# Kernel tuning notes

Hardware: AMD Instinct MI355X
Metric: run time of the kernel (lower is better)

The kernel has to match this reference:

```python
import jax, jax.numpy as jnp
import numpy as np

KERNEL = (7, 7)
NUM_CH = 4
EPS = 1e-06
ROPE_BASE = 10000.0


def _rel_dist():
    coords = [np.arange(k, dtype=np.float32) - k // 2 for k in KERNEL]
    g = np.meshgrid(*coords, indexing='ij')
    d = np.sqrt(sum(gi ** 2 for gi in g))
    return jnp.asarray(d.reshape(-1)), float(d.max())


def silu(x):
    return x * jax.nn.sigmoid(x)


def rmsnorm(x, w):
    rms = jnp.sqrt(jnp.mean(x * x, axis=-1, keepdims=True) + EPS)
    return x / rms * w


def apply_rope(x):
    # x: (B, L, H, D); positions run over dim -2 (matches torch default)
    H, D = x.shape[-2], x.shape[-1]
    half = D // 2
    pos = jnp.arange(H, dtype=jnp.float32)
    freqs = 1.0 / (ROPE_BASE ** (jnp.arange(half, dtype=x.dtype) / half))
    ang = pos[:, None] * freqs  # (H, half)
    cos, sin = jnp.cos(ang), jnp.sin(ang)
    x1, x2 = x[..., :half], x[..., half:2 * half]
    return jnp.concatenate([x1 * cos - x2 * sin, x1 * sin + x2 * cos], axis=-1)


def unfold2d(x):
    # x: (B, Hs, Ws, C) -> (B, Hs, Ws, k1*k2, C), row-major kernel order
    B, Hs, Ws, C = x.shape
    k1, k2 = KERNEL
    xp = jnp.pad(x, ((0, 0), ((k1 - 1) // 2, k1 // 2), ((k2 - 1) // 2, k2 // 2), (0, 0)))
    wins = [xp[:, i:i + Hs, j:j + Ws, :] for i in range(k1) for j in range(k2)]
    return jnp.stack(wins, axis=3)


def setup_inputs() -> dict:
    key = jax.random.key(0)
    ks = jax.random.split(key, 8)
    C = 256
    x = jax.random.normal(ks[0], (2, 64, 64, C), dtype=jnp.float32)
    W_qkv = jax.random.normal(ks[1], (C, 3 * C), dtype=jnp.float32) * 0.02
    w_qnorm = jnp.ones((C // NUM_CH,), dtype=jnp.float32)
    w_knorm = jnp.ones((C // NUM_CH,), dtype=jnp.float32)
    W_wp = jax.random.normal(ks[2], (C, 2 * NUM_CH), dtype=jnp.float32) * 0.02
    b_wp = jax.random.normal(ks[3], (2 * NUM_CH,), dtype=jnp.float32) * 0.02
    w_onorm = jnp.ones((C,), dtype=jnp.float32)
    W_out = jax.random.normal(ks[4], (C, C), dtype=jnp.float32) * 0.02
    W_gate = jax.random.normal(ks[5], (C, C), dtype=jnp.float32) * 0.02
    b_gate = 2.0 * jnp.ones((C,), dtype=jnp.float32)
    return {"x": x, "W_qkv": W_qkv, "w_qnorm": w_qnorm, "w_knorm": w_knorm,
            "W_wp": W_wp, "b_wp": b_wp, "w_onorm": w_onorm, "W_out": W_out,
            "W_gate": W_gate, "b_gate": b_gate}


def reference(x, W_qkv, w_qnorm, w_knorm, W_wp, b_wp, w_onorm, W_out, W_gate, b_gate):
    rel_dist, max_dist = _rel_dist()
    B, Hs, Ws, C = x.shape
    L = Hs * Ws
    H = NUM_CH
    D = C // H
    Wsz = KERNEL[0] * KERNEL[1]
    scale = D ** (-0.5)

    qkv = silu(x @ W_qkv)
    q, k, v = jnp.split(qkv, 3, axis=-1)

    q_flat = apply_rope(rmsnorm(q.reshape(B, L, H, D), w_qnorm))
    k_flat = apply_rope(rmsnorm(k.reshape(B, L, H, D), w_knorm))
    k = k_flat.reshape(B, Hs, Ws, C)

    wp = silu(x @ W_wp + b_wp)  # (B, Hs, Ws, 2H)
    width_raw, sharp_raw = jnp.split(wp, 2, axis=-1)
    width = jax.nn.sigmoid(width_raw) * max_dist + 0.5
    sharpness = jax.nn.sigmoid(sharp_raw) * 9.5 + 0.5

    k_win = unfold2d(k).reshape(B, L, Wsz, H, D)
    v_win = unfold2d(v).reshape(B, L, Wsz, H, D)

    scores = jnp.einsum('blhd,blwhd->blhw', q_flat, k_win) * scale
    width_f = width.reshape(B, L, H, 1)
    sharp_f = sharpness.reshape(B, L, H, 1)
    soft_mask = jax.nn.sigmoid((width_f - rel_dist) * sharp_f)
    scores = scores - (1.0 - soft_mask) * 10000.0
    attn = jax.nn.softmax(scores, axis=-1)

    out = jnp.einsum('blhw,blwhd->blhd', attn, v_win).reshape(B, Hs, Ws, C)
    out = rmsnorm(out, w_onorm)

    gate = jax.nn.sigmoid(silu(v @ W_gate + b_gate))
    merged = gate * v + (1.0 - gate) * out
    return silu(merged @ W_out)
```

## Files before the change

kernel.cpp:

```cpp
#include <hip/hip_runtime.h>
#include <hip/hip_fp16.h>
#include <math.h>

__device__ __forceinline__ float sigm(float x)  { return 1.0f / (1.0f + __expf(-x)); }
__device__ __forceinline__ float siluf(float x) { return x * sigm(x); }

typedef _Float16 half8  __attribute__((ext_vector_type(8)));
typedef _Float16 half4  __attribute__((ext_vector_type(4)));
typedef float    f32x4  __attribute__((ext_vector_type(4)));

__device__ __forceinline__ void gld16(const void* g, void* l) {
    __builtin_amdgcn_global_load_lds(
        (const __attribute__((address_space(1))) unsigned*)g,
        (__attribute__((address_space(3))) unsigned*)l, 16, 0, 0);
}

template <int MI, int AMODE>
__device__ __forceinline__ void gemm_core16(
    const __half* __restrict__ A16,
    const __half* __restrict__ Bhi, const __half* __restrict__ Blo,
    int nbs, int m0, int n0, int t, f32x4 (&acc)[MI][4])
{
    __shared__ short As[MI * 1024], BsHi[4096], BsLo[4096];
    const int lane = t & 63, wave = t >> 6;
    const int wm = (wave >> 1) * (MI << 4), wn = (wave & 1) << 6;
    const int fr = lane & 15, fq = lane >> 4;

    for (int kb = 0; kb < 8; ++kb) {
        __syncthreads();
#pragma unroll
        for (int hf = 0; hf < MI / 2; ++hf) {
            const int rr = wave * (MI << 3) + (hf << 4);
            size_t ga;
            if (AMODE == 0)
                ga = (((size_t)(kb * 8192 + m0 + rr)) << 5) + (lane << 3);
            else
                ga = (((size_t)(m0 + rr + (lane >> 2))) << 8) + (kb << 5) + ((lane & 3) << 3);
            gld16(A16 + ga, &As[rr << 5]);
        }
#pragma unroll
        for (int hf = 0; hf < 2; ++hf) {
            const int rr = (wave << 5) + (hf << 4);
            const size_t gb = (((size_t)(kb * nbs + n0 + rr)) << 5) + (lane << 3);
            gld16(Bhi + gb, &BsHi[rr << 5]);
            gld16(Blo + gb, &BsLo[rr << 5]);
        }
        __syncthreads();

        half8 a[MI], bh[4], bl[4];
#pragma unroll
        for (int i = 0; i < MI; ++i)
            a[i] = *(const half8*)&As[((wm + (i << 4) + fr) << 5) + (fq << 3)];
#pragma unroll
        for (int i = 0; i < 4; ++i) {
            const int boff = ((wn + (i << 4) + fr) << 5) + (fq << 3);
            bh[i] = *(const half8*)&BsHi[boff];
            bl[i] = *(const half8*)&BsLo[boff];
        }
#pragma unroll
        for (int mi = 0; mi < MI; ++mi)
#pragma unroll
            for (int ni = 0; ni < 4; ++ni) {
                acc[mi][ni] = __builtin_amdgcn_mfma_f32_16x16x32_f16(a[mi], bh[ni], acc[mi][ni], 0, 0, 0);
                acc[mi][ni] = __builtin_amdgcn_mfma_f32_16x16x32_f16(a[mi], bl[ni], acc[mi][ni], 0, 0, 0);
            }
    }
}

__global__ __launch_bounds__(256) void prep_kernel(
    const float* __restrict__ x, const float* __restrict__ Wqkv,
    const float* __restrict__ Wgate, const float* __restrict__ Wout,
    const float* __restrict__ Wwp, const float* __restrict__ bwp,
    __half* __restrict__ xh,
    __half* __restrict__ wqh, __half* __restrict__ wql,
    __half* __restrict__ wgh, __half* __restrict__ wgl,
    __half* __restrict__ woh, __half* __restrict__ wol,
    float* __restrict__ width, float* __restrict__ sharp)
{
    __shared__ float xs[32][260];
    const int t = threadIdx.x;
    const int blk = blockIdx.x;
    if (blk < 256) {
        const int row0 = blk << 5;
        for (int e = t; e < 2048; e += 256) {
            int r = e >> 6, cc = (e & 63) << 2;
            *(float4*)&xs[r][cc] = *(const float4*)&x[(size_t)(row0 + r) * 256 + cc];
        }
        __syncthreads();
        const int r = t >> 3, kb = t & 7;
        __half hibuf[32];
#pragma unroll
        for (int i = 0; i < 32; ++i)
            hibuf[i] = __float2half(xs[r][(kb << 5) + i]);
        const size_t ob = ((size_t)(kb * 8192 + row0 + r)) << 5;
#pragma unroll
        for (int i = 0; i < 4; ++i)
            *(int4*)&xh[ob + (i << 3)] = *(int4*)&hibuf[i << 3];
        float acc = 0.f;
#pragma unroll 8
        for (int k = 0; k < 256; ++k) acc += xs[r][k] * Wwp[k * 8 + kb];
        float s = sigm(siluf(acc + bwp[kb]));
        const int row = row0 + r;
        if (kb < 4) width[row * 4 + kb] = s * 4.242640687119285f + 0.5f;
        else        sharp[row * 4 + kb - 4] = s * 9.5f + 0.5f;
    } else {
        const float* W; __half *Whi, *Wlo; int N, nb0, ncnt;
        if (blk < 288)      { W = Wqkv;  Whi = wqh; Wlo = wql; N = 768; nb0 = (blk - 256) * 24; ncnt = 24; }
        else if (blk < 296) { W = Wgate; Whi = wgh; Wlo = wgl; N = 256; nb0 = (blk - 288) * 32; ncnt = 32; }
        else                { W = Wout;  Whi = woh; Wlo = wol; N = 256; nb0 = (blk - 296) * 32; ncnt = 32; }
        for (int j = 0; j < ncnt; ++j)
            xs[j][t] = W[(size_t)t * N + nb0 + j];
        __syncthreads();
        for (int c = t; c < ncnt * 8; c += 256) {
            const int j = c >> 3, kb = c & 7;
            __half hibuf[32], lobuf[32];
#pragma unroll
            for (int i = 0; i < 32; ++i) {
                float v = xs[j][(kb << 5) + i];
                __half hv = __float2half(v);
                hibuf[i] = hv;
                lobuf[i] = __float2half(v - __half2float(hv));
            }
            const size_t ob = ((size_t)(kb * N + nb0 + j)) << 5;
#pragma unroll
            for (int i = 0; i < 4; ++i) {
                *(int4*)&Whi[ob + (i << 3)] = *(int4*)&hibuf[i << 3];
                *(int4*)&Wlo[ob + (i << 3)] = *(int4*)&lobuf[i << 3];
            }
        }
    }
}

__global__ __launch_bounds__(256, 3) void gemm_qkv(
    const __half* __restrict__ xh,
    const __half* __restrict__ wqh, const __half* __restrict__ wql,
    const float* __restrict__ wq, const float* __restrict__ wk,
    __half* __restrict__ qh, __half* __restrict__ kh, __half* __restrict__ vh)
{
    const int t  = threadIdx.x;
    const int m0 = blockIdx.y << 7, n0 = blockIdx.x << 7;
    f32x4 acc[4][4] = {};
    gemm_core16<4, 0>(xh, wqh, wql, 768, m0, n0, t, acc);

    const int lane = t & 63, wave = t >> 6;
    const int wm = (wave >> 1) << 6, wn = (wave & 1) << 6;
    const int fr = lane & 15, fq = lane >> 4;
    const int gc0 = n0 + wn;
    const int seg = gc0 >> 8;
    const int h   = (gc0 >> 6) & 3;
    const int hc0 = h << 6;

#pragma unroll
    for (int mi = 0; mi < 4; ++mi)
#pragma unroll
        for (int ni = 0; ni < 4; ++ni)
#pragma unroll
            for (int r = 0; r < 4; ++r)
                acc[mi][ni][r] = siluf(acc[mi][ni][r]);

    if (seg == 2) {
#pragma unroll
        for (int mi = 0; mi < 4; ++mi)
#pragma unroll
            for (int r = 0; r < 4; ++r) {
                const size_t row = m0 + wm + (mi << 4) + (fq << 2) + r;
#pragma unroll
                for (int ni = 0; ni < 4; ++ni)
                    vh[row * 256 + hc0 + (ni << 4) + fr] = __float2half(acc[mi][ni][r]);
            }
    } else {
        const float* wnorm = seg ? wk : wq;
        float wv[4];
#pragma unroll
        for (int ni = 0; ni < 4; ++ni) wv[ni] = wnorm[(ni << 4) + fr];
        float cs[2], sn[2];
#pragma unroll
        for (int j = 0; j < 2; ++j) {
            const int d = (j << 4) + fr;
            const float freq = powf(10000.f, -(float)d * (1.f / 32.f));
            const float ang = (float)h * freq;
            cs[j] = cosf(ang); sn[j] = sinf(ang);
        }
        __half* dstbase = (seg ? kh : qh);
#pragma unroll
        for (int mi = 0; mi < 4; ++mi)
#pragma unroll
            for (int r = 0; r < 4; ++r) {
                float ss = acc[mi][0][r] * acc[mi][0][r] + acc[mi][1][r] * acc[mi][1][r]
                         + acc[mi][2][r] * acc[mi][2][r] + acc[mi][3][r] * acc[mi][3][r];
                ss += __shfl_xor(ss, 1); ss += __shfl_xor(ss, 2);
                ss += __shfl_xor(ss, 4); ss += __shfl_xor(ss, 8);
                const float rinv = 1.f / sqrtf(ss * (1.f / 64.f) + 1e-6f);
                float xv[4];
#pragma unroll
                for (int ni = 0; ni < 4; ++ni) xv[ni] = acc[mi][ni][r] * rinv * wv[ni];
                const float o0 = xv[0] * cs[0] - xv[2] * sn[0];
                const float o2 = xv[0] * sn[0] + xv[2] * cs[0];
                const float o1 = xv[1] * cs[1] - xv[3] * sn[1];
                const float o3 = xv[1] * sn[1] + xv[3] * cs[1];
                const size_t row = m0 + wm + (mi << 4) + (fq << 2) + r;
                __half* dst = dstbase + row * 256 + hc0;
                dst[fr]      = __float2half(o0);
                dst[16 + fr] = __float2half(o1);
                dst[32 + fr] = __float2half(o2);
                dst[48 + fr] = __float2half(o3);
            }
    }
}

__global__ __launch_bounds__(256, 3) void gemm_gate(
    const __half* __restrict__ vh,
    const __half* __restrict__ wgh, const __half* __restrict__ wgl,
    const float* __restrict__ bias, const float* __restrict__ attn_o,
    const float* __restrict__ sumsq4, const float* __restrict__ w_onorm,
    __half* __restrict__ mh)
{
    const int t  = threadIdx.x;
    const int m0 = blockIdx.y << 6, n0 = blockIdx.x << 7;
    f32x4 acc[2][4] = {};
    gemm_core16<2, 1>(vh, wgh, wgl, 256, m0, n0, t, acc);

    const int lane = t & 63, wave = t >> 6;
    const int wm = (wave >> 1) << 5, wn = (wave & 1) << 6;
    const int fr = lane & 15, fq = lane >> 4;

    float rmsf[2][4];
#pragma unroll
    for (int mi = 0; mi < 2; ++mi)
#pragma unroll
        for (int r = 0; r < 4; ++r) {
            const int m = m0 + wm + (mi << 4) + (fq << 2) + r;
            float4 s4 = *(const float4*)&sumsq4[(size_t)m * 4];
            rmsf[mi][r] = 1.f / sqrtf((s4.x + s4.y + s4.z + s4.w) * (1.f / 256.f) + 1e-6f);
        }

#pragma unroll
    for (int mi = 0; mi < 2; ++mi)
#pragma unroll
        for (int ni = 0; ni < 4; ++ni) {
            const int n  = n0 + wn + (ni << 4) + fr;
            const int mb = m0 + wm + (mi << 4) + (fq << 2);
            const float bb  = bias[n];
            const float won = w_onorm[n];
#pragma unroll
            for (int r = 0; r < 4; ++r) {
                const int m = mb + r;
                const float g  = sigm(siluf(acc[mi][ni][r] + bb));
                const float vv = __half2float(vh[(size_t)m * 256 + n]);
                const float oo = attn_o[(size_t)m * 256 + n] * rmsf[mi][r] * won;
                mh[(size_t)m * 256 + n] = __float2half(g * vv + (1.f - g) * oo);
            }
        }
}

__global__ __launch_bounds__(256, 3) void gemm_out(
    const __half* __restrict__ mh,
    const __half* __restrict__ woh, const __half* __restrict__ wol,
    float* __restrict__ out)
{
    const int t  = threadIdx.x;
    const int m0 = blockIdx.y << 6, n0 = blockIdx.x << 7;
    f32x4 acc[2][4] = {};
    gemm_core16<2, 1>(mh, woh, wol, 256, m0, n0, t, acc);

    const int lane = t & 63, wave = t >> 6;
    const int wm = (wave >> 1) << 5, wn = (wave & 1) << 6;
    const int fr = lane & 15, fq = lane >> 4;
#pragma unroll
    for (int mi = 0; mi < 2; ++mi)
#pragma unroll
        for (int ni = 0; ni < 4; ++ni) {
            const int n  = n0 + wn + (ni << 4) + fr;
            const int mb = m0 + wm + (mi << 4) + (fq << 2);
#pragma unroll
            for (int r = 0; r < 4; ++r)
                out[(size_t)(mb + r) * 256 + n] = siluf(acc[mi][ni][r]);
        }
}

#define PTV 208
#define PTP 112

__global__ __launch_bounds__(256, 4) void attn_mfma(
    const __half* __restrict__ qh, const __half* __restrict__ kh,
    const __half* __restrict__ vh, const float* __restrict__ width,
    const float* __restrict__ sharp, float* __restrict__ attn_o,
    float* __restrict__ sumsq4)
{
    __shared__ short smem[20480];
    short* Vt  = smem;
    short* Psh = smem + 13312;

    const int t = threadIdx.x;
    const int lane = t & 63, wave = t >> 6;
    const int fr = lane & 15, fq = lane >> 4;
    const int patch = blockIdx.x, h = blockIdx.y, b = blockIdx.z;
    const int pr0 = (patch >> 3) << 3, pc0 = (patch & 7) << 3;
    const size_t cb0 = ((size_t)b << 20) + ((size_t)h << 6);

    float wd[4], sh[4]; int lq[4];
#pragma unroll
    for (int r = 0; r < 4; ++r) {
        const int q = (wave << 4) + (fq << 2) + r;
        lq[r] = (pr0 + (q >> 3)) * 64 + pc0 + (q & 7);
        wd[r] = width[((b << 12) + lq[r]) * 4 + h];
        sh[r] = sharp[((b << 12) + lq[r]) * 4 + h];
    }

    const int srow = t >> 5;
    const int d2 = (t & 31) << 1;
    unsigned v0[13], v1[13];
#pragma unroll
    for (int j = 0; j < 13; ++j) {
        const int p = (j << 4) + (srow << 1);
#pragma unroll
        for (int e = 0; e < 2; ++e) {
            const int pp = p + e;
            const int pi = pp / 14, pj = pp - pi * 14;
            const int gr = pr0 - 3 + pi, gc = pc0 - 3 + pj;
            const bool ok = (pp < 196) & ((unsigned)gr < 64u) & ((unsigned)gc < 64u);
            const int grc = min(max(gr, 0), 63), gcc = min(max(gc, 0), 63);
            const unsigned vv = *(const unsigned*)(vh + cb0 + (size_t)((grc << 6) + gcc) * 256 + d2);
            (e ? v1 : v0)[j] = ok ? vv : 0u;
        }
    }
#pragma unroll
    for (int j = 0; j < 13; ++j) {
        const int p = (j << 4) + (srow << 1);
        const unsigned lo = (v0[j] & 0xffffu) | (v1[j] << 16);
        const unsigned hi = (v0[j] >> 16) | (v1[j] & 0xffff0000u);
        *(unsigned*)&Vt[d2 * PTV + p]       = lo;
        *(unsigned*)&Vt[(d2 + 1) * PTV + p] = hi;
    }

    const int qrow = (wave << 4) + fr;
    const int lqr = (pr0 + (qrow >> 3)) * 64 + pc0 + (qrow & 7);
    const __half* qptr = qh + cb0 + (size_t)lqr * 256 + (fq << 3);
    half8 a0 = *(const half8*)qptr;
    half8 a1 = *(const half8*)(qptr + 32);

    f32x4 sc[13];
#define KADDR(tl) ({                                                        \
        const int p_ = ((tl) << 4) + fr;                                    \
        const int pi_ = p_ / 14, pj_ = p_ - pi_ * 14;                       \
        const int grc_ = min(max(pr0 - 3 + pi_, 0), 63);                    \
        const int gcc_ = min(max(pc0 - 3 + pj_, 0), 63);                    \
        kh + cb0 + (size_t)((grc_ << 6) + gcc_) * 256 + (fq << 3); })

    half8 k0a[5], k0b[5];
#pragma unroll
    for (int i = 0; i < 5; ++i) {
        const __half* kp = KADDR(i);
        k0a[i] = *(const half8*)kp; k0b[i] = *(const half8*)(kp + 32);
    }
    half8 k1a[4], k1b[4];
#pragma unroll
    for (int i = 0; i < 4; ++i) {
        const __half* kp = KADDR(5 + i);
        k1a[i] = *(const half8*)kp; k1b[i] = *(const half8*)(kp + 32);
    }
#pragma unroll
    for (int i = 0; i < 5; ++i) {
        f32x4 z = {0.f, 0.f, 0.f, 0.f};
        z = __builtin_amdgcn_mfma_f32_16x16x32_f16(a0, k0a[i], z, 0, 0, 0);
        sc[i] = __builtin_amdgcn_mfma_f32_16x16x32_f16(a1, k0b[i], z, 0, 0, 0);
    }
    half8 k2a[4], k2b[4];
#pragma unroll
    for (int i = 0; i < 4; ++i) {
        const __half* kp = KADDR(9 + i);
        k2a[i] = *(const half8*)kp; k2b[i] = *(const half8*)(kp + 32);
    }
#pragma unroll
    for (int i = 0; i < 4; ++i) {
        f32x4 z = {0.f, 0.f, 0.f, 0.f};
        z = __builtin_amdgcn_mfma_f32_16x16x32_f16(a0, k1a[i], z, 0, 0, 0);
        sc[5 + i] = __builtin_amdgcn_mfma_f32_16x16x32_f16(a1, k1b[i], z, 0, 0, 0);
    }
#pragma unroll
    for (int i = 0; i < 4; ++i) {
        f32x4 z = {0.f, 0.f, 0.f, 0.f};
        z = __builtin_amdgcn_mfma_f32_16x16x32_f16(a0, k2a[i], z, 0, 0, 0);
        sc[9 + i] = __builtin_amdgcn_mfma_f32_16x16x32_f16(a1, k2b[i], z, 0, 0, 0);
    }
#undef KADDR

    float mx[4] = {-3e38f, -3e38f, -3e38f, -3e38f};
#pragma unroll
    for (int tl = 0; tl < 13; ++tl) {
        const int p = (tl << 4) + fr;
        const int pi = p / 14, pj = p - pi * 14;
        const bool pvld = p < 196;
        const bool inb = pvld & ((unsigned)(pr0 - 3 + pi) < 64u) & ((unsigned)(pc0 - 3 + pj) < 64u);
#pragma unroll
        for (int r = 0; r < 4; ++r) {
            const int q = (wave << 4) + (fq << 2) + r;
            const int di = pi - 3 - ((q >> 3) & 7), dj = pj - 3 - (q & 7);
            const bool win = pvld & ((unsigned)(di + 3) <= 6u) & ((unsigned)(dj + 3) <= 6u);
            const float rel = sqrtf((float)(di * di + dj * dj));
            const float mk = sigm((wd[r] - rel) * sh[r]);
            const float s0 = inb ? sc[tl][r] * 0.125f : 0.f;
            float s = s0 - (1.f - mk) * 10000.f;
            s = win ? s : -3e38f;
            sc[tl][r] = s;
            mx[r] = fmaxf(mx[r], s);
        }
    }
#pragma unroll
    for (int r = 0; r < 4; ++r) {
        mx[r] = fmaxf(mx[r], __shfl_xor(mx[r], 1));
        mx[r] = fmaxf(mx[r], __shfl_xor(mx[r], 2));
        mx[r] = fmaxf(mx[r], __shfl_xor(mx[r], 4));
        mx[r] = fmaxf(mx[r], __shfl_xor(mx[r], 8));
    }
    float sm[4] = {0.f, 0.f, 0.f, 0.f};
#pragma unroll
    for (int tl = 0; tl < 13; ++tl)
#pragma unroll
        for (int r = 0; r < 4; ++r) {
            const float e = __expf(sc[tl][r] - mx[r]);
            sc[tl][r] = e; sm[r] += e;
        }
#pragma unroll
    for (int r = 0; r < 4; ++r) {
        sm[r] += __shfl_xor(sm[r], 1);
        sm[r] += __shfl_xor(sm[r], 2);
        sm[r] += __shfl_xor(sm[r], 4);
        sm[r] += __shfl_xor(sm[r], 8);
        sm[r] = 1.f / sm[r];
    }

#pragma unroll
    for (int tl = 0; tl < 7; ++tl)
#pragma unroll
        for (int r = 0; r < 4; ++r) {
            __half pv = __float2half(sc[tl][r] * sm[r]);
            Psh[((wave << 4) + (fq << 2) + r) * PTP + (tl << 4) + fr] = *(short*)&pv;
        }
    __syncthreads();

    f32x4 o[4] = {};
    const int pra = (wave << 4) + fr;
#pragma unroll
    for (int s = 0; s < 3; ++s) {
        half8 pa = *(const half8*)&Psh[pra * PTP + (fq << 3) + (s << 5)];
#pragma unroll
        for (int dt = 0; dt < 4; ++dt) {
            half8 vbf = *(const half8*)&Vt[((dt << 4) + fr) * PTV + (fq << 3) + (s << 5)];
            o[dt] = __builtin_amdgcn_mfma_f32_16x16x32_f16(pa, vbf, o[dt], 0, 0, 0);
        }
    }
    {
        half4 pa = *(const half4*)&Psh[pra * PTP + 96 + (fq << 2)];
#pragma unroll
        for (int dt = 0; dt < 4; ++dt) {
            half4 vbf = *(const half4*)&Vt[((dt << 4) + fr) * PTV + 96 + (fq << 2)];
            o[dt] = __builtin_amdgcn_mfma_f32_16x16x16f16(pa, vbf, o[dt], 0, 0, 0);
        }
    }

    __syncthreads();

#pragma unroll
    for (int tl = 7; tl < 13; ++tl)
#pragma unroll
        for (int r = 0; r < 4; ++r) {
            __half pv = __float2half(sc[tl][r] * sm[r]);
            Psh[((wave << 4) + (fq << 2) + r) * PTP + ((tl - 7) << 4) + fr] = *(short*)&pv;
        }
    asm volatile("s_waitcnt lgkmcnt(0)" ::: "memory");

#pragma unroll
    for (int s = 0; s < 3; ++s) {
        half8 pa = *(const half8*)&Psh[pra * PTP + (fq << 3) + (s << 5)];
#pragma unroll
        for (int dt = 0; dt < 4; ++dt) {
            half8 vbf = *(const half8*)&Vt[((dt << 4) + fr) * PTV + 112 + (fq << 3) + (s << 5)];
            o[dt] = __builtin_amdgcn_mfma_f32_16x16x32_f16(pa, vbf, o[dt], 0, 0, 0);
        }
    }

#pragma unroll
    for (int r = 0; r < 4; ++r) {
        float ss = o[0][r]*o[0][r] + o[1][r]*o[1][r] + o[2][r]*o[2][r] + o[3][r]*o[3][r];
        ss += __shfl_xor(ss, 1); ss += __shfl_xor(ss, 2);
        ss += __shfl_xor(ss, 4); ss += __shfl_xor(ss, 8);
        const size_t rowb = (((size_t)(b << 12) + lq[r]) << 8) + h * 64;
#pragma unroll
        for (int dt = 0; dt < 4; ++dt)
            attn_o[rowb + (dt << 4) + fr] = o[dt][r];
        if (fr == 0) sumsq4[(((b << 12) + lq[r]) << 2) + h] = ss;
    }
}

extern "C" void kernel_launch(void* const* d_in, const int* in_sizes, int n_in,
                              void* d_out, int out_size, void* d_ws, size_t ws_size,
                              hipStream_t stream)
{
    const float* x      = (const float*)d_in[0];
    const float* W_qkv  = (const float*)d_in[1];
    const float* w_qn   = (const float*)d_in[2];
    const float* w_kn   = (const float*)d_in[3];
    const float* W_wp   = (const float*)d_in[4];
    const float* b_wp   = (const float*)d_in[5];
    const float* w_on   = (const float*)d_in[6];
    const float* W_out  = (const float*)d_in[7];
    const float* W_gate = (const float*)d_in[8];
    const float* b_gate = (const float*)d_in[9];
    float* out = (float*)d_out;

    __half* ws16 = (__half*)d_ws;
    __half* xh  = ws16;
    __half* wqh = xh  + 2097152;
    __half* wql = wqh + 196608;
    __half* wgh = wql + 196608;
    __half* wgl = wgh + 65536;
    __half* woh = wgl + 65536;
    __half* wol = woh + 65536;
    __half* qhp = wol + 65536;
    __half* khp = qhp + 2097152;
    __half* vhp = khp + 2097152;
    __half* mh  = vhp + 2097152;
    float* attn_o = (float*)(mh + 2097152);
    float* widthp = attn_o + 2097152;
    float* sharpp = widthp + 32768;
    float* sumsq4 = sharpp + 32768;

    prep_kernel<<<304, 256, 0, stream>>>(x, W_qkv, W_gate, W_out, W_wp, b_wp,
                                         xh, wqh, wql, wgh, wgl, woh, wol,
                                         widthp, sharpp);
    gemm_qkv<<<dim3(6, 64), 256, 0, stream>>>(xh, wqh, wql, w_qn, w_kn,
                                              qhp, khp, vhp);
    attn_mfma<<<dim3(64, 4, 2), 256, 0, stream>>>(qhp, khp, vhp, widthp, sharpp,
                                                  attn_o, sumsq4);
    gemm_gate<<<dim3(2, 128), 256, 0, stream>>>(vhp, wgh, wgl, b_gate,
                                                attn_o, sumsq4, w_on, mh);
    gemm_out<<<dim3(2, 128), 256, 0, stream>>>(mh, woh, wol, out);
}
```

Measured before the change: 164.5 us.

## Process two K-blocks per sync in GEMM core and store attention output as fp16

The shared GEMM core now loads two K-slices into doubled LDS buffers per barrier pair and computes both, halving the number of synchronisations per tile. Separately, the attention kernel writes its unnormalised output in half precision and the gate kernel reads it as half, halving that intermediate's traffic. The cost is larger LDS use per block, which may lower occupancy, and some precision loss in the intermediate before RMS normalisation.

```diff
diff --git a/kernel.cpp b/kernel.cpp
--- a/kernel.cpp
+++ b/kernel.cpp
@@ -21,49 +21,56 @@
     const __half* __restrict__ Bhi, const __half* __restrict__ Blo,
     int nbs, int m0, int n0, int t, f32x4 (&acc)[MI][4])
 {
-    __shared__ short As[MI * 1024], BsHi[4096], BsLo[4096];
+    __shared__ short As[2 * MI * 1024], BsHi[2 * 4096], BsLo[2 * 4096];
     const int lane = t & 63, wave = t >> 6;
     const int wm = (wave >> 1) * (MI << 4), wn = (wave & 1) << 6;
     const int fr = lane & 15, fq = lane >> 4;
 
-    for (int kb = 0; kb < 8; ++kb) {
+    for (int kb2 = 0; kb2 < 4; ++kb2) {
         __syncthreads();
 #pragma unroll
-        for (int hf = 0; hf < MI / 2; ++hf) {
-            const int rr = wave * (MI << 3) + (hf << 4);
-            size_t ga;
-            if (AMODE == 0)
-                ga = (((size_t)(kb * 8192 + m0 + rr)) << 5) + (lane << 3);
-            else
-                ga = (((size_t)(m0 + rr + (lane >> 2))) << 8) + (kb << 5) + ((lane & 3) << 3);
-            gld16(A16 + ga, &As[rr << 5]);
-        }
-#pragma unroll
-        for (int hf = 0; hf < 2; ++hf) {
-            const int rr = (wave << 5) + (hf << 4);
-            const size_t gb = (((size_t)(kb * nbs + n0 + rr)) << 5) + (lane << 3);
-            gld16(Bhi + gb, &BsHi[rr << 5]);
-            gld16(Blo + gb, &BsLo[rr << 5]);
+        for (int s = 0; s < 2; ++s) {
+            const int kb = (kb2 << 1) + s;
+#pragma unroll
+            for (int hf = 0; hf < MI / 2; ++hf) {
+                const int rr = wave * (MI << 3) + (hf << 4);
+                size_t ga;
+                if (AMODE == 0)
+                    ga = (((size_t)(kb * 8192 + m0 + rr)) << 5) + (lane << 3);
+                else
+                    ga = (((size_t)(m0 + rr + (lane >> 2))) << 8) + (kb << 5) + ((lane & 3) << 3);
+                gld16(A16 + ga, &As[s * MI * 1024 + (rr << 5)]);
+            }
+#pragma unroll
+            for (int hf = 0; hf < 2; ++hf) {
+                const int rr = (wave << 5) + (hf << 4);
+                const size_t gb = (((size_t)(kb * nbs + n0 + rr)) << 5) + (lane << 3);
+                gld16(Bhi + gb, &BsHi[s * 4096 + (rr << 5)]);
+                gld16(Blo + gb, &BsLo[s * 4096 + (rr << 5)]);
+            }
         }
         __syncthreads();
 
-        half8 a[MI], bh[4], bl[4];
-#pragma unroll
-        for (int i = 0; i < MI; ++i)
-            a[i] = *(const half8*)&As[((wm + (i << 4) + fr) << 5) + (fq << 3)];
-#pragma unroll
-        for (int i = 0; i < 4; ++i) {
-            const int boff = ((wn + (i << 4) + fr) << 5) + (fq << 3);
-            bh[i] = *(const half8*)&BsHi[boff];
-            bl[i] = *(const half8*)&BsLo[boff];
-        }
-#pragma unroll
-        for (int mi = 0; mi < MI; ++mi)
-#pragma unroll
-            for (int ni = 0; ni < 4; ++ni) {
-                acc[mi][ni] = __builtin_amdgcn_mfma_f32_16x16x32_f16(a[mi], bh[ni], acc[mi][ni], 0, 0, 0);
-                acc[mi][ni] = __builtin_amdgcn_mfma_f32_16x16x32_f16(a[mi], bl[ni], acc[mi][ni], 0, 0, 0);
-            }
+#pragma unroll
+        for (int s = 0; s < 2; ++s) {
+            half8 a[MI], bh[4], bl[4];
+#pragma unroll
+            for (int i = 0; i < MI; ++i)
+                a[i] = *(const half8*)&As[s * MI * 1024 + ((wm + (i << 4) + fr) << 5) + (fq << 3)];
+#pragma unroll
+            for (int i = 0; i < 4; ++i) {
+                const int boff = s * 4096 + ((wn + (i << 4) + fr) << 5) + (fq << 3);
+                bh[i] = *(const half8*)&BsHi[boff];
+                bl[i] = *(const half8*)&BsLo[boff];
+            }
+#pragma unroll
+            for (int mi = 0; mi < MI; ++mi)
+#pragma unroll
+                for (int ni = 0; ni < 4; ++ni) {
+                    acc[mi][ni] = __builtin_amdgcn_mfma_f32_16x16x32_f16(a[mi], bh[ni], acc[mi][ni], 0, 0, 0);
+                    acc[mi][ni] = __builtin_amdgcn_mfma_f32_16x16x32_f16(a[mi], bl[ni], acc[mi][ni], 0, 0, 0);
+                }
+        }
     }
 }
 
@@ -211,7 +218,7 @@
 __global__ __launch_bounds__(256, 3) void gemm_gate(
     const __half* __restrict__ vh,
     const __half* __restrict__ wgh, const __half* __restrict__ wgl,
-    const float* __restrict__ bias, const float* __restrict__ attn_o,
+    const float* __restrict__ bias, const __half* __restrict__ attn_o,
     const float* __restrict__ sumsq4, const float* __restrict__ w_onorm,
     __half* __restrict__ mh)
 {
@@ -247,7 +254,7 @@
                 const int m = mb + r;
                 const float g  = sigm(siluf(acc[mi][ni][r] + bb));
                 const float vv = __half2float(vh[(size_t)m * 256 + n]);
-                const float oo = attn_o[(size_t)m * 256 + n] * rmsf[mi][r] * won;
+                const float oo = __half2float(attn_o[(size_t)m * 256 + n]) * rmsf[mi][r] * won;
                 mh[(size_t)m * 256 + n] = __float2half(g * vv + (1.f - g) * oo);
             }
         }
@@ -284,7 +291,7 @@
 __global__ __launch_bounds__(256, 4) void attn_mfma(
     const __half* __restrict__ qh, const __half* __restrict__ kh,
     const __half* __restrict__ vh, const float* __restrict__ width,
-    const float* __restrict__ sharp, float* __restrict__ attn_o,
+    const float* __restrict__ sharp, __half* __restrict__ attn_o,
     float* __restrict__ sumsq4)
 {
     __shared__ short smem[20480];
@@ -488,7 +495,7 @@
         const size_t rowb = (((size_t)(b << 12) + lq[r]) << 8) + h * 64;
 #pragma unroll
         for (int dt = 0; dt < 4; ++dt)
-            attn_o[rowb + (dt << 4) + fr] = o[dt][r];
+            attn_o[rowb + (dt << 4) + fr] = __float2half(o[dt][r]);
         if (fr == 0) sumsq4[(((b << 12) + lq[r]) << 2) + h] = ss;
     }
 }
@@ -521,8 +528,8 @@
     __half* khp = qhp + 2097152;
     __half* vhp = khp + 2097152;
     __half* mh  = vhp + 2097152;
-    float* attn_o = (float*)(mh + 2097152);
-    float* widthp = attn_o + 2097152;
+    __half* attn_o = mh + 2097152;
+    float* widthp = (float*)(attn_o + 2097152);
     float* sharpp = widthp + 32768;
     float* sumsq4 = sharpp + 32768;
 
```

New measurement: 159.3 us. -3.2%, faster.
